# Optimization experiments

Hardware: AMD Instinct MI355X
Metric: run time of the kernel (lower is better)

The kernel has to match this reference:

```python
import jax, jax.numpy as jnp
import numpy as np

B = 512
D_IN = 64
D_MODEL = 768
DEPTH = 24
D_INNER = 1536   # expand=2 * d_model
D_STATE = 16
D_CONV = 4
DT_RANK = 48     # ceil(d_model/16)


def setup_inputs() -> dict:
    key = jax.random.key(0)
    ks = jax.random.split(key, 12)
    s = 0.02
    x_t = jax.random.normal(ks[0], (B, 1, D_IN), dtype=jnp.float32)
    in_w = jax.random.normal(ks[1], (D_MODEL, D_IN), dtype=jnp.float32) * s
    in_b = jnp.zeros((D_MODEL,), jnp.float32)
    xz_w = jax.random.normal(ks[2], (DEPTH, 2 * D_INNER, D_MODEL), dtype=jnp.float32) * s
    conv_w = jax.random.normal(ks[3], (DEPTH, D_INNER, D_CONV), dtype=jnp.float32) * s
    conv_b = jnp.zeros((DEPTH, D_INNER), jnp.float32)
    xproj_w = jax.random.normal(ks[4], (DEPTH, DT_RANK + 2 * D_STATE, D_INNER), dtype=jnp.float32) * s
    dtproj_w = jax.random.normal(ks[5], (DEPTH, D_INNER, DT_RANK), dtype=jnp.float32) * s
    # dt bias initialized so softplus(dt) ~ [1e-3, 1e-1], as in mamba_ssm
    dtproj_b = jax.random.uniform(ks[6], (DEPTH, D_INNER), minval=-4.6, maxval=-2.3)
    # A = arange(1, d_state+1) per channel -> A_log = log(A)
    A_log = jnp.broadcast_to(jnp.log(jnp.arange(1, D_STATE + 1, dtype=jnp.float32)),
                             (DEPTH, D_INNER, D_STATE)).copy()
    D = jnp.ones((DEPTH, D_INNER), jnp.float32)
    outproj_w = jax.random.normal(ks[7], (DEPTH, D_MODEL, D_INNER), dtype=jnp.float32) * s
    conv_state = jax.random.normal(ks[8], (DEPTH, B, D_INNER, D_CONV), dtype=jnp.float32) * 0.1
    ssm_state = jax.random.normal(ks[9], (DEPTH, B, D_INNER, D_STATE), dtype=jnp.float32) * 0.1
    ln_g = jnp.ones((D_MODEL,), jnp.float32)
    ln_b = jnp.zeros((D_MODEL,), jnp.float32)
    return dict(x_t=x_t, in_w=in_w, in_b=in_b, xz_w=xz_w, conv_w=conv_w, conv_b=conv_b,
                xproj_w=xproj_w, dtproj_w=dtproj_w, dtproj_b=dtproj_b, A_log=A_log, D=D,
                outproj_w=outproj_w, conv_state=conv_state, ssm_state=ssm_state,
                ln_g=ln_g, ln_b=ln_b)


def _layer_step(h, layer):
    """One Mamba selective-scan decode step for a single layer. h: (B, D_INNER*... wait (B, d_model))"""
    (xz_w, conv_w, conv_b, xproj_w, dtproj_w, dtproj_b, A_log, Dp, outproj_w, cs, ss) = layer
    xz = h @ xz_w.T                                  # (B, 2*d_inner)
    x, z = jnp.split(xz, 2, axis=-1)                 # (B, d_inner) each
    # causal conv1d cache update: shift left, append new token
    cs = jnp.concatenate([cs[..., 1:], x[..., None]], axis=-1)   # (B, d_inner, d_conv)
    x = jnp.sum(cs * conv_w[None], axis=-1) + conv_b             # (B, d_inner)
    x = jax.nn.silu(x)
    xdb = x @ xproj_w.T                              # (B, dt_rank + 2*d_state)
    dt = xdb[:, :DT_RANK] @ dtproj_w.T               # (B, d_inner)
    Bm = xdb[:, DT_RANK:DT_RANK + D_STATE]           # (B, d_state)
    C = xdb[:, DT_RANK + D_STATE:]                   # (B, d_state)
    dt = jax.nn.softplus(dt + dtproj_b)
    A = -jnp.exp(A_log)                              # (d_inner, d_state)
    dA = jnp.exp(dt[:, :, None] * A[None])           # (B, d_inner, d_state)
    ss = ss * dA + (dt * x)[:, :, None] * Bm[:, None, :]
    y = jnp.einsum('bdn,bn->bd', ss, C) + Dp * x
    y = y * jax.nn.silu(z)
    h = y @ outproj_w.T                              # (B, d_model)
    return h, None


def reference(x_t, in_w, in_b, xz_w, conv_w, conv_b, xproj_w, dtproj_w, dtproj_b,
              A_log, D, outproj_w, conv_state, ssm_state, ln_g, ln_b):
    h = x_t[:, 0, :] @ in_w.T + in_b                 # (B, d_model)
    h, _ = jax.lax.scan(_layer_step, h,
                        (xz_w, conv_w, conv_b, xproj_w, dtproj_w, dtproj_b,
                         A_log, D, outproj_w, conv_state, ssm_state))
    mu = jnp.mean(h, axis=-1, keepdims=True)
    var = jnp.var(h, axis=-1, keepdims=True)
    h = (h - mu) / jnp.sqrt(var + 1e-5) * ln_g + ln_b
    return h[:, None, :]                             # (B, 1, d_model)
```

## Files before the change

### kernel.cpp

```cpp
#include <hip/hip_runtime.h>
#include <cstdint>
#include <cstddef>

#define BATCH 512
#define D_IN 64
#define D_MODEL 768
#define DEPTH 24
#define D_INNER 1536
#define D_STATE 16
#define D_CONV 4
#define DT_RANK 48
#define XDB_DIM 80

typedef __bf16 bf16x8 __attribute__((ext_vector_type(8)));
typedef unsigned short ushortx8 __attribute__((ext_vector_type(8)));
typedef float f32x4 __attribute__((ext_vector_type(4)));

__device__ __forceinline__ float sigmoidf_(float v) { return 1.f / (1.f + expf(-v)); }

__device__ __forceinline__ void split1(float f, unsigned short& h, unsigned short& l) {
    unsigned int u = __float_as_uint(f);
    unsigned int uh = u & 0xffff0000u;
    h = (unsigned short)(uh >> 16);
    float r = f - __uint_as_float(uh);
    l = (unsigned short)(__float_as_uint(r) >> 16);
}

template<bool CONV>
__global__ __launch_bounds__(256) void mfma_gemm(
    const float* __restrict__ A,
    const float* __restrict__ W,
    float* __restrict__ Cout,
    float* __restrict__ Zout,
    const float* __restrict__ conv_state,
    const float* __restrict__ conv_w,
    const float* __restrict__ conv_b,
    int N, int K)
{
    __shared__ __align__(16) unsigned short As[2][64 * 64];
    __shared__ __align__(16) unsigned short Bs[2][64 * 64];

    const int t = threadIdx.x;
    const int bn0 = blockIdx.x * 64;
    const int bm0 = blockIdx.y * 64;
    const int sr = t >> 2;
    const int sc = (t & 3) << 3;
    const int lane = t & 63;
    const int wv = t >> 6;
    const int wm = wv >> 1, wn = wv & 1;
    const int ln15 = lane & 15, kq = lane >> 4;

    const float* Aptr = A + (size_t)(bm0 + sr) * K + sc;
    const float* Wptr = W + (size_t)(bn0 + sr) * K + sc;

    f32x4 acc[2][2];
#pragma unroll
    for (int m = 0; m < 2; ++m)
#pragma unroll
        for (int n = 0; n < 2; ++n) acc[m][n] = (f32x4){0.f, 0.f, 0.f, 0.f};

    auto stage = [&](float4 x0, float4 x1, unsigned short* S) {
        float f[8] = {x0.x, x0.y, x0.z, x0.w, x1.x, x1.y, x1.z, x1.w};
        ushortx8 hi, lo;
#pragma unroll
        for (int j = 0; j < 8; ++j) {
            unsigned short h, l;
            split1(f[j], h, l);
            hi[j] = h; lo[j] = l;
        }
        const int s0 = sc >> 3;
        const int sw = sr & 7;
        *(ushortx8*)&S[sr * 64 + ((s0 ^ sw) << 3)] = hi;
        *(ushortx8*)&S[sr * 64 + (((s0 + 4) ^ sw) << 3)] = lo;
    };

    const int nk = K >> 5;

    float4 a0 = *(const float4*)(Aptr);
    float4 a1 = *(const float4*)(Aptr + 4);
    float4 b0 = *(const float4*)(Wptr);
    float4 b1 = *(const float4*)(Wptr + 4);
    stage(a0, a1, As[0]);
    stage(b0, b1, Bs[0]);

    for (int kb = 0; kb < nk; ++kb) {
        __syncthreads();
        const int cur = kb & 1;
        if (kb + 1 < nk) {
            const float* Ap = Aptr + ((kb + 1) << 5);
            const float* Wp = Wptr + ((kb + 1) << 5);
            a0 = *(const float4*)(Ap);
            a1 = *(const float4*)(Ap + 4);
            b0 = *(const float4*)(Wp);
            b1 = *(const float4*)(Wp + 4);
        }
        bf16x8 ah[2], al[2], bh[2], bl[2];
#pragma unroll
        for (int m = 0; m < 2; ++m) {
            const int r = wm * 32 + m * 16 + ln15;
            const int base = r * 64;
            const int sw = r & 7;
            ah[m] = __builtin_bit_cast(bf16x8, *(ushortx8*)&As[cur][base + ((kq ^ sw) << 3)]);
            al[m] = __builtin_bit_cast(bf16x8, *(ushortx8*)&As[cur][base + (((kq + 4) ^ sw) << 3)]);
        }
#pragma unroll
        for (int n = 0; n < 2; ++n) {
            const int r = wn * 32 + n * 16 + ln15;
            const int base = r * 64;
            const int sw = r & 7;
            bh[n] = __builtin_bit_cast(bf16x8, *(ushortx8*)&Bs[cur][base + ((kq ^ sw) << 3)]);
            bl[n] = __builtin_bit_cast(bf16x8, *(ushortx8*)&Bs[cur][base + (((kq + 4) ^ sw) << 3)]);
        }
#pragma unroll
        for (int m = 0; m < 2; ++m)
#pragma unroll
            for (int n = 0; n < 2; ++n) {
                acc[m][n] = __builtin_amdgcn_mfma_f32_16x16x32_bf16(ah[m], bh[n], acc[m][n], 0, 0, 0);
                acc[m][n] = __builtin_amdgcn_mfma_f32_16x16x32_bf16(ah[m], bl[n], acc[m][n], 0, 0, 0);
                acc[m][n] = __builtin_amdgcn_mfma_f32_16x16x32_bf16(al[m], bh[n], acc[m][n], 0, 0, 0);
            }
        if (kb + 1 < nk) {
            stage(a0, a1, As[cur ^ 1]);
            stage(b0, b1, Bs[cur ^ 1]);
        }
    }

#pragma unroll
    for (int m = 0; m < 2; ++m) {
#pragma unroll
        for (int n = 0; n < 2; ++n) {
            const int col = bn0 + wn * 32 + n * 16 + ln15;
            const int row0 = bm0 + wm * 32 + m * 16 + kq * 4;
            f32x4 v = acc[m][n];
            if (CONV) {
                if (col < D_INNER) {
                    const float4 cwv = *(const float4*)(conv_w + (size_t)col * 4);
                    const float cbv = conv_b[col];
#pragma unroll
                    for (int j = 0; j < 4; ++j) {
                        const int row = row0 + j;
                        const float4 csv = *(const float4*)(conv_state + ((size_t)row * D_INNER + col) * 4);
                        float c = csv.y * cwv.x + csv.z * cwv.y + csv.w * cwv.z
                                + v[j] * cwv.w + cbv;
                        Cout[(size_t)row * D_INNER + col] = c * sigmoidf_(c);
                    }
                } else {
#pragma unroll
                    for (int j = 0; j < 4; ++j)
                        Zout[(size_t)(row0 + j) * D_INNER + (col - D_INNER)] = v[j];
                }
            } else {
#pragma unroll
                for (int j = 0; j < 4; ++j)
                    Cout[(size_t)(row0 + j) * N + col] = v[j];
            }
        }
    }
}

template<int TM, int TN, bool BIAS>
__global__ __launch_bounds__(256) void gemm_k(
    const float* __restrict__ A,
    const float* __restrict__ W,
    const float* __restrict__ bias,
    float* __restrict__ Cout,
    int M, int N, int K)
{
    constexpr int BM = 16 * TM;
    constexpr int BN = 16 * TN;
    constexpr int BK = 16;
    __shared__ float As[BK][BM + 4];
    __shared__ float Ws[BK][BN + 4];

    const int tid = threadIdx.x;
    const int tx = tid & 15;
    const int ty = tid >> 4;
    const int bn0 = blockIdx.x * BN;
    const int bm0 = blockIdx.y * BM;

    float acc[TM][TN];
#pragma unroll
    for (int i = 0; i < TM; ++i)
#pragma unroll
        for (int j = 0; j < TN; ++j) acc[i][j] = 0.f;

    for (int k0 = 0; k0 < K; k0 += BK) {
        {
            int r = tid >> 2, c = (tid & 3) << 2;
            float4 a4 = *(const float4*)(A + (size_t)(bm0 + r) * K + k0 + c);
            As[c + 0][r] = a4.x; As[c + 1][r] = a4.y;
            As[c + 2][r] = a4.z; As[c + 3][r] = a4.w;
            float4 w4 = *(const float4*)(W + (size_t)(bn0 + r) * K + k0 + c);
            Ws[c + 0][r] = w4.x; Ws[c + 1][r] = w4.y;
            Ws[c + 2][r] = w4.z; Ws[c + 3][r] = w4.w;
        }
        __syncthreads();
#pragma unroll
        for (int kk = 0; kk < BK; ++kk) {
            float af[TM], wf[TN];
#pragma unroll
            for (int i = 0; i < TM; ++i) af[i] = As[kk][ty * TM + i];
#pragma unroll
            for (int j = 0; j < TN; ++j) wf[j] = Ws[kk][tx * TN + j];
#pragma unroll
            for (int i = 0; i < TM; ++i)
#pragma unroll
                for (int j = 0; j < TN; ++j) acc[i][j] += af[i] * wf[j];
        }
        __syncthreads();
    }

#pragma unroll
    for (int i = 0; i < TM; ++i) {
        const int bb = bm0 + ty * TM + i;
#pragma unroll
        for (int j = 0; j < TN; ++j) {
            const int n = bn0 + tx * TN + j;
            float v = acc[i][j];
            if (BIAS) v += bias[n];
            Cout[(size_t)bb * N + n] = v;
        }
    }
}

__global__ __launch_bounds__(256) void bc_kernel(
    const float* __restrict__ x,
    const float* __restrict__ z,
    const float* __restrict__ xproj_w,
    const float* __restrict__ dtproj_w,
    const float* __restrict__ dtproj_b,
    const float* __restrict__ A_log,
    const float* __restrict__ Dp,
    const float* __restrict__ ssm,
    float* __restrict__ y)
{
    const int b = blockIdx.x;
    const int tid = threadIdx.x;
    __shared__ __align__(16) float xs[D_INNER];
    __shared__ float xdb[XDB_DIM];

    const float4* xrow = (const float4*)(x + (size_t)b * D_INNER);
    float4* xs4 = (float4*)xs;
    for (int i = tid; i < D_INNER / 4; i += 256) xs4[i] = xrow[i];
    __syncthreads();

    const int lane = tid & 63;
    const int wv = tid >> 6;
    for (int n = wv; n < XDB_DIM; n += 4) {
        const float4* wr = (const float4*)(xproj_w + (size_t)n * D_INNER);
        float s = 0.f;
#pragma unroll
        for (int j = 0; j < D_INNER / 4 / 64; ++j) {
            float4 w = wr[lane + 64 * j];
            float4 xv = xs4[lane + 64 * j];
            s += w.x * xv.x + w.y * xv.y + w.z * xv.z + w.w * xv.w;
        }
#pragma unroll
        for (int off = 32; off > 0; off >>= 1) s += __shfl_xor(s, off);
        if (lane == 0) xdb[n] = s;
    }
    __syncthreads();

    float Bmv[D_STATE], Cv[D_STATE];
#pragma unroll
    for (int n = 0; n < D_STATE; ++n) {
        Bmv[n] = xdb[DT_RANK + n];
        Cv[n] = xdb[DT_RANK + D_STATE + n];
    }

    for (int d = tid; d < D_INNER; d += 256) {
        const float4* dtw = (const float4*)(dtproj_w + (size_t)d * DT_RANK);
        float s = 0.f;
#pragma unroll
        for (int j = 0; j < DT_RANK / 4; ++j) {
            float4 w = dtw[j];
            s += w.x * xdb[4 * j + 0] + w.y * xdb[4 * j + 1]
               + w.z * xdb[4 * j + 2] + w.w * xdb[4 * j + 3];
        }
        s += dtproj_b[d];
        float dt = fmaxf(s, 0.f) + log1pf(expf(-fabsf(s)));
        float xv = xs[d];
        float dtx = dt * xv;

        const float4* ssp = (const float4*)(ssm + ((size_t)b * D_INNER + d) * D_STATE);
        const float4* alp = (const float4*)(A_log + (size_t)d * D_STATE);
        float yacc = 0.f;
#pragma unroll
        for (int q = 0; q < 4; ++q) {
            float4 al = alp[q];
            float4 sv = ssp[q];
            float e0 = expf(-dt * expf(al.x));
            float e1 = expf(-dt * expf(al.y));
            float e2 = expf(-dt * expf(al.z));
            float e3 = expf(-dt * expf(al.w));
            yacc += (sv.x * e0 + dtx * Bmv[4 * q + 0]) * Cv[4 * q + 0];
            yacc += (sv.y * e1 + dtx * Bmv[4 * q + 1]) * Cv[4 * q + 1];
            yacc += (sv.z * e2 + dtx * Bmv[4 * q + 2]) * Cv[4 * q + 2];
            yacc += (sv.w * e3 + dtx * Bmv[4 * q + 3]) * Cv[4 * q + 3];
        }
        yacc += Dp[d] * xv;
        float zv = z[(size_t)b * D_INNER + d];
        y[(size_t)b * D_INNER + d] = yacc * (zv * sigmoidf_(zv));
    }
}

__global__ __launch_bounds__(256) void ln_kernel(
    const float* __restrict__ h, const float* __restrict__ g,
    const float* __restrict__ be, float* __restrict__ out)
{
    const int b = blockIdx.x;
    const int tid = threadIdx.x;
    float v[3];
#pragma unroll
    for (int j = 0; j < 3; ++j) v[j] = h[(size_t)b * D_MODEL + tid + j * 256];
    float s = v[0] + v[1] + v[2];
    float s2 = v[0] * v[0] + v[1] * v[1] + v[2] * v[2];
#pragma unroll
    for (int off = 32; off > 0; off >>= 1) {
        s += __shfl_xor(s, off);
        s2 += __shfl_xor(s2, off);
    }
    __shared__ float red[8];
    const int lane = tid & 63, wv = tid >> 6;
    if (lane == 0) { red[wv] = s; red[4 + wv] = s2; }
    __syncthreads();
    s = red[0] + red[1] + red[2] + red[3];
    s2 = red[4] + red[5] + red[6] + red[7];
    const float mu = s * (1.f / D_MODEL);
    const float var = s2 * (1.f / D_MODEL) - mu * mu;
    const float inv = 1.f / sqrtf(var + 1e-5f);
#pragma unroll
    for (int j = 0; j < 3; ++j) {
        int c = tid + j * 256;
        out[(size_t)b * D_MODEL + c] = (v[j] - mu) * inv * g[c] + be[c];
    }
}

extern "C" void kernel_launch(void* const* d_in, const int* in_sizes, int n_in,
                              void* d_out, int out_size, void* d_ws, size_t ws_size,
                              hipStream_t stream)
{
    const float* x_t        = (const float*)d_in[0];
    const float* in_w       = (const float*)d_in[1];
    const float* in_b       = (const float*)d_in[2];
    const float* xz_w       = (const float*)d_in[3];
    const float* conv_w     = (const float*)d_in[4];
    const float* conv_b     = (const float*)d_in[5];
    const float* xproj_w    = (const float*)d_in[6];
    const float* dtproj_w   = (const float*)d_in[7];
    const float* dtproj_b   = (const float*)d_in[8];
    const float* A_log      = (const float*)d_in[9];
    const float* Dvec       = (const float*)d_in[10];
    const float* outproj_w  = (const float*)d_in[11];
    const float* conv_state = (const float*)d_in[12];
    const float* ssm_state  = (const float*)d_in[13];
    const float* ln_g       = (const float*)d_in[14];
    const float* ln_b       = (const float*)d_in[15];

    float* ws = (float*)d_ws;
    float* h = ws;
    float* x = h + (size_t)BATCH * D_MODEL;
    float* z = x + (size_t)BATCH * D_INNER;
    float* y = z + (size_t)BATCH * D_INNER;

    dim3 blk(256);

    gemm_k<4, 4, true><<<dim3(D_MODEL / 64, BATCH / 64), blk, 0, stream>>>(
        x_t, in_w, in_b, h, BATCH, D_MODEL, D_IN);

    for (int l = 0; l < DEPTH; ++l) {
        const float* xzw = xz_w + (size_t)l * 2 * D_INNER * D_MODEL;
        const float* csl = conv_state + (size_t)l * BATCH * D_INNER * D_CONV;
        const float* cwl = conv_w + (size_t)l * D_INNER * D_CONV;
        const float* cbl = conv_b + (size_t)l * D_INNER;
        const float* xpl = xproj_w + (size_t)l * XDB_DIM * D_INNER;
        const float* dwl = dtproj_w + (size_t)l * D_INNER * DT_RANK;
        const float* dbl = dtproj_b + (size_t)l * D_INNER;
        const float* all = A_log + (size_t)l * D_INNER * D_STATE;
        const float* dpl = Dvec + (size_t)l * D_INNER;
        const float* ssl = ssm_state + (size_t)l * BATCH * D_INNER * D_STATE;
        const float* opl = outproj_w + (size_t)l * D_MODEL * D_INNER;

        mfma_gemm<true><<<dim3(2 * D_INNER / 64, BATCH / 64), blk, 0, stream>>>(
            h, xzw, x, z, csl, cwl, cbl, 2 * D_INNER, D_MODEL);

        bc_kernel<<<dim3(BATCH), blk, 0, stream>>>(
            x, z, xpl, dwl, dbl, all, dpl, ssl, y);

        mfma_gemm<false><<<dim3(D_MODEL / 64, BATCH / 64), blk, 0, stream>>>(
            y, opl, h, nullptr, nullptr, nullptr, nullptr, D_MODEL, D_INNER);
    }

    ln_kernel<<<dim3(BATCH), blk, 0, stream>>>(h, ln_g, ln_b, (float*)d_out);
}
```

Before: 2.663 ms.

## Pre-split weights and activations into bf16 hi/lo planes before MFMA GEMMs

Adds a prep kernel that converts the xz and out-projection weights into separate bf16 hi/lo arrays once per call. Producer kernels (input GEMM, bc_kernel, out-projection GEMM) now also write the hi/lo split of their fp32 outputs. The MFMA GEMM loads ready-made bf16 halves instead of splitting fp32 in its staging loop. This removes per-tile conversion ALU work, but each call pays a full pass over the weights (reading about 226 MB of fp32 and writing the same in bf16), plus extra output stores.

```diff
diff --git a/kernel.cpp b/kernel.cpp
--- a/kernel.cpp
+++ b/kernel.cpp
@@ -15,6 +15,7 @@
 typedef __bf16 bf16x8 __attribute__((ext_vector_type(8)));
 typedef unsigned short ushortx8 __attribute__((ext_vector_type(8)));
 typedef float f32x4 __attribute__((ext_vector_type(4)));
+typedef unsigned short ushort_t;
 
 __device__ __forceinline__ float sigmoidf_(float v) { return 1.f / (1.f + expf(-v)); }
 
@@ -26,12 +27,36 @@
     l = (unsigned short)(__float_as_uint(r) >> 16);
 }
 
+__global__ __launch_bounds__(256) void prep_split(
+    const float* __restrict__ src, ushort_t* __restrict__ hi, ushort_t* __restrict__ lo,
+    long n8)
+{
+    long i = (long)blockIdx.x * 256 + threadIdx.x;
+    const long stride = (long)gridDim.x * 256;
+    for (; i < n8; i += stride) {
+        float4 a = *(const float4*)(src + i * 8);
+        float4 b = *(const float4*)(src + i * 8 + 4);
+        float f[8] = {a.x, a.y, a.z, a.w, b.x, b.y, b.z, b.w};
+        ushortx8 h, l;
+#pragma unroll
+        for (int j = 0; j < 8; ++j) {
+            unsigned short hh, ll;
+            split1(f[j], hh, ll);
+            h[j] = hh; l[j] = ll;
+        }
+        *(ushortx8*)(hi + i * 8) = h;
+        *(ushortx8*)(lo + i * 8) = l;
+    }
+}
+
 template<bool CONV>
-__global__ __launch_bounds__(256) void mfma_gemm(
-    const float* __restrict__ A,
-    const float* __restrict__ W,
+__global__ __launch_bounds__(256) void mfma_gemm2(
+    const ushort_t* __restrict__ Ahi, const ushort_t* __restrict__ Alo,
+    const ushort_t* __restrict__ Whi, const ushort_t* __restrict__ Wlo,
     float* __restrict__ Cout,
     float* __restrict__ Zout,
+    ushort_t* __restrict__ Chi,
+    ushort_t* __restrict__ Clo,
     const float* __restrict__ conv_state,
     const float* __restrict__ conv_w,
     const float* __restrict__ conv_b,
@@ -44,14 +69,16 @@
     const int bn0 = blockIdx.x * 64;
     const int bm0 = blockIdx.y * 64;
     const int sr = t >> 2;
-    const int sc = (t & 3) << 3;
+    const int s0 = t & 3;
     const int lane = t & 63;
     const int wv = t >> 6;
     const int wm = wv >> 1, wn = wv & 1;
     const int ln15 = lane & 15, kq = lane >> 4;
 
-    const float* Aptr = A + (size_t)(bm0 + sr) * K + sc;
-    const float* Wptr = W + (size_t)(bn0 + sr) * K + sc;
+    const ushort_t* Ah = Ahi + (size_t)(bm0 + sr) * K + s0 * 8;
+    const ushort_t* Al = Alo + (size_t)(bm0 + sr) * K + s0 * 8;
+    const ushort_t* Wh = Whi + (size_t)(bn0 + sr) * K + s0 * 8;
+    const ushort_t* Wl = Wlo + (size_t)(bn0 + sr) * K + s0 * 8;
 
     f32x4 acc[2][2];
 #pragma unroll
@@ -59,57 +86,47 @@
 #pragma unroll
         for (int n = 0; n < 2; ++n) acc[m][n] = (f32x4){0.f, 0.f, 0.f, 0.f};
 
-    auto stage = [&](float4 x0, float4 x1, unsigned short* S) {
-        float f[8] = {x0.x, x0.y, x0.z, x0.w, x1.x, x1.y, x1.z, x1.w};
-        ushortx8 hi, lo;
-#pragma unroll
-        for (int j = 0; j < 8; ++j) {
-            unsigned short h, l;
-            split1(f[j], h, l);
-            hi[j] = h; lo[j] = l;
-        }
-        const int s0 = sc >> 3;
-        const int sw = sr & 7;
+    const int sw = sr & 7;
+    auto stage = [&](ushortx8 hi, ushortx8 lo, unsigned short* S) {
         *(ushortx8*)&S[sr * 64 + ((s0 ^ sw) << 3)] = hi;
         *(ushortx8*)&S[sr * 64 + (((s0 + 4) ^ sw) << 3)] = lo;
     };
 
     const int nk = K >> 5;
 
-    float4 a0 = *(const float4*)(Aptr);
-    float4 a1 = *(const float4*)(Aptr + 4);
-    float4 b0 = *(const float4*)(Wptr);
-    float4 b1 = *(const float4*)(Wptr + 4);
-    stage(a0, a1, As[0]);
-    stage(b0, b1, Bs[0]);
+    ushortx8 pah = *(const ushortx8*)Ah;
+    ushortx8 pal = *(const ushortx8*)Al;
+    ushortx8 pwh = *(const ushortx8*)Wh;
+    ushortx8 pwl = *(const ushortx8*)Wl;
+    stage(pah, pal, As[0]);
+    stage(pwh, pwl, Bs[0]);
 
     for (int kb = 0; kb < nk; ++kb) {
         __syncthreads();
         const int cur = kb & 1;
         if (kb + 1 < nk) {
-            const float* Ap = Aptr + ((kb + 1) << 5);
-            const float* Wp = Wptr + ((kb + 1) << 5);
-            a0 = *(const float4*)(Ap);
-            a1 = *(const float4*)(Ap + 4);
-            b0 = *(const float4*)(Wp);
-            b1 = *(const float4*)(Wp + 4);
+            const int ko = (kb + 1) << 5;
+            pah = *(const ushortx8*)(Ah + ko);
+            pal = *(const ushortx8*)(Al + ko);
+            pwh = *(const ushortx8*)(Wh + ko);
+            pwl = *(const ushortx8*)(Wl + ko);
         }
         bf16x8 ah[2], al[2], bh[2], bl[2];
 #pragma unroll
         for (int m = 0; m < 2; ++m) {
             const int r = wm * 32 + m * 16 + ln15;
             const int base = r * 64;
-            const int sw = r & 7;
-            ah[m] = __builtin_bit_cast(bf16x8, *(ushortx8*)&As[cur][base + ((kq ^ sw) << 3)]);
-            al[m] = __builtin_bit_cast(bf16x8, *(ushortx8*)&As[cur][base + (((kq + 4) ^ sw) << 3)]);
+            const int rs = r & 7;
+            ah[m] = __builtin_bit_cast(bf16x8, *(ushortx8*)&As[cur][base + ((kq ^ rs) << 3)]);
+            al[m] = __builtin_bit_cast(bf16x8, *(ushortx8*)&As[cur][base + (((kq + 4) ^ rs) << 3)]);
         }
 #pragma unroll
         for (int n = 0; n < 2; ++n) {
             const int r = wn * 32 + n * 16 + ln15;
             const int base = r * 64;
-            const int sw = r & 7;
-            bh[n] = __builtin_bit_cast(bf16x8, *(ushortx8*)&Bs[cur][base + ((kq ^ sw) << 3)]);
-            bl[n] = __builtin_bit_cast(bf16x8, *(ushortx8*)&Bs[cur][base + (((kq + 4) ^ sw) << 3)]);
+            const int rs = r & 7;
+            bh[n] = __builtin_bit_cast(bf16x8, *(ushortx8*)&Bs[cur][base + ((kq ^ rs) << 3)]);
+            bl[n] = __builtin_bit_cast(bf16x8, *(ushortx8*)&Bs[cur][base + (((kq + 4) ^ rs) << 3)]);
         }
 #pragma unroll
         for (int m = 0; m < 2; ++m)
@@ -120,8 +137,8 @@
                 acc[m][n] = __builtin_amdgcn_mfma_f32_16x16x32_bf16(al[m], bh[n], acc[m][n], 0, 0, 0);
             }
         if (kb + 1 < nk) {
-            stage(a0, a1, As[cur ^ 1]);
-            stage(b0, b1, Bs[cur ^ 1]);
+            stage(pah, pal, As[cur ^ 1]);
+            stage(pwh, pwl, Bs[cur ^ 1]);
         }
     }
 
@@ -151,19 +168,27 @@
                 }
             } else {
 #pragma unroll
-                for (int j = 0; j < 4; ++j)
-                    Cout[(size_t)(row0 + j) * N + col] = v[j];
+                for (int j = 0; j < 4; ++j) {
+                    const size_t idx = (size_t)(row0 + j) * N + col;
+                    float val = v[j];
+                    Cout[idx] = val;
+                    unsigned short hh, ll;
+                    split1(val, hh, ll);
+                    Chi[idx] = hh;
+                    Clo[idx] = ll;
+                }
             }
         }
     }
 }
 
-template<int TM, int TN, bool BIAS>
+template<int TM, int TN>
 __global__ __launch_bounds__(256) void gemm_k(
     const float* __restrict__ A,
     const float* __restrict__ W,
     const float* __restrict__ bias,
     float* __restrict__ Cout,
+    ushort_t* __restrict__ Chi, ushort_t* __restrict__ Clo,
     int M, int N, int K)
 {
     constexpr int BM = 16 * TM;
@@ -216,9 +241,13 @@
 #pragma unroll
         for (int j = 0; j < TN; ++j) {
             const int n = bn0 + tx * TN + j;
-            float v = acc[i][j];
-            if (BIAS) v += bias[n];
-            Cout[(size_t)bb * N + n] = v;
+            float v = acc[i][j] + bias[n];
+            const size_t idx = (size_t)bb * N + n;
+            Cout[idx] = v;
+            unsigned short hh, ll;
+            split1(v, hh, ll);
+            Chi[idx] = hh;
+            Clo[idx] = ll;
         }
     }
 }
@@ -232,7 +261,8 @@
     const float* __restrict__ A_log,
     const float* __restrict__ Dp,
     const float* __restrict__ ssm,
-    float* __restrict__ y)
+    float* __restrict__ y,
+    ushort_t* __restrict__ yhi, ushort_t* __restrict__ ylo)
 {
     const int b = blockIdx.x;
     const int tid = threadIdx.x;
@@ -300,7 +330,13 @@
         }
         yacc += Dp[d] * xv;
         float zv = z[(size_t)b * D_INNER + d];
-        y[(size_t)b * D_INNER + d] = yacc * (zv * sigmoidf_(zv));
+        float out = yacc * (zv * sigmoidf_(zv));
+        const size_t idx = (size_t)b * D_INNER + d;
+        y[idx] = out;
+        unsigned short hh, ll;
+        split1(out, hh, ll);
+        yhi[idx] = hh;
+        ylo[idx] = ll;
     }
 }
 
@@ -362,14 +398,31 @@
     float* x = h + (size_t)BATCH * D_MODEL;
     float* z = x + (size_t)BATCH * D_INNER;
     float* y = z + (size_t)BATCH * D_INNER;
+    ushort_t* us = (ushort_t*)(y + (size_t)BATCH * D_INNER);
+    ushort_t* h_hi   = us;
+    ushort_t* h_lo   = h_hi + (size_t)BATCH * D_MODEL;
+    ushort_t* y_hi   = h_lo + (size_t)BATCH * D_MODEL;
+    ushort_t* y_lo   = y_hi + (size_t)BATCH * D_INNER;
+    ushort_t* xzw_hi = y_lo + (size_t)BATCH * D_INNER;
+    ushort_t* xzw_lo = xzw_hi + (size_t)DEPTH * 2 * D_INNER * D_MODEL;
+    ushort_t* opw_hi = xzw_lo + (size_t)DEPTH * 2 * D_INNER * D_MODEL;
+    ushort_t* opw_lo = opw_hi + (size_t)DEPTH * D_MODEL * D_INNER;
 
     dim3 blk(256);
 
-    gemm_k<4, 4, true><<<dim3(D_MODEL / 64, BATCH / 64), blk, 0, stream>>>(
-        x_t, in_w, in_b, h, BATCH, D_MODEL, D_IN);
+    prep_split<<<dim3(2048), blk, 0, stream>>>(
+        xz_w, xzw_hi, xzw_lo, (long)DEPTH * 2 * D_INNER * D_MODEL / 8);
+    prep_split<<<dim3(2048), blk, 0, stream>>>(
+        outproj_w, opw_hi, opw_lo, (long)DEPTH * D_MODEL * D_INNER / 8);
+
+    gemm_k<4, 4><<<dim3(D_MODEL / 64, BATCH / 64), blk, 0, stream>>>(
+        x_t, in_w, in_b, h, h_hi, h_lo, BATCH, D_MODEL, D_IN);
 
     for (int l = 0; l < DEPTH; ++l) {
-        const float* xzw = xz_w + (size_t)l * 2 * D_INNER * D_MODEL;
+        const ushort_t* xzh = xzw_hi + (size_t)l * 2 * D_INNER * D_MODEL;
+        const ushort_t* xzl = xzw_lo + (size_t)l * 2 * D_INNER * D_MODEL;
+        const ushort_t* oph = opw_hi + (size_t)l * D_MODEL * D_INNER;
+        const ushort_t* opl = opw_lo + (size_t)l * D_MODEL * D_INNER;
         const float* csl = conv_state + (size_t)l * BATCH * D_INNER * D_CONV;
         const float* cwl = conv_w + (size_t)l * D_INNER * D_CONV;
         const float* cbl = conv_b + (size_t)l * D_INNER;
@@ -379,16 +432,17 @@
         const float* all = A_log + (size_t)l * D_INNER * D_STATE;
         const float* dpl = Dvec + (size_t)l * D_INNER;
         const float* ssl = ssm_state + (size_t)l * BATCH * D_INNER * D_STATE;
-        const float* opl = outproj_w + (size_t)l * D_MODEL * D_INNER;
-
-        mfma_gemm<true><<<dim3(2 * D_INNER / 64, BATCH / 64), blk, 0, stream>>>(
-            h, xzw, x, z, csl, cwl, cbl, 2 * D_INNER, D_MODEL);
+
+        mfma_gemm2<true><<<dim3(2 * D_INNER / 64, BATCH / 64), blk, 0, stream>>>(
+            h_hi, h_lo, xzh, xzl, x, z, nullptr, nullptr,
+            csl, cwl, cbl, 2 * D_INNER, D_MODEL);
 
         bc_kernel<<<dim3(BATCH), blk, 0, stream>>>(
-            x, z, xpl, dwl, dbl, all, dpl, ssl, y);
-
-        mfma_gemm<false><<<dim3(D_MODEL / 64, BATCH / 64), blk, 0, stream>>>(
-            y, opl, h, nullptr, nullptr, nullptr, nullptr, D_MODEL, D_INNER);
+            x, z, xpl, dwl, dbl, all, dpl, ssl, y, y_hi, y_lo);
+
+        mfma_gemm2<false><<<dim3(D_MODEL / 64, BATCH / 64), blk, 0, stream>>>(
+            y_hi, y_lo, oph, opl, h, nullptr, h_hi, h_lo,
+            nullptr, nullptr, nullptr, D_MODEL, D_INNER);
     }
 
     ln_kernel<<<dim3(BATCH), blk, 0, stream>>>(h, ln_g, ln_b, (float*)d_out);
```

Result: faster. 2.467 ms (-7.4%).
